# Optimization experiments

Hardware: AMD Instinct MI355X
Metric: run time of the kernel (lower is better)

## Reference

```python
import jax, jax.numpy as jnp
import numpy as np

MARGIN = 1.0  # config['margin']


def setup_inputs() -> dict:
    key = jax.random.key(0)
    k1, k2 = jax.random.split(key)
    features = jax.random.normal(k1, (1024, 512), dtype=jnp.float32)
    labels = jax.random.randint(k2, (1024,), 0, 32)
    return {"features": features, "labels": labels}


def _cdist(x):
    # Pairwise euclidean distances, matching torch.cdist; zero-distance
    # entries (e.g., the diagonal) get zero gradient like torch's backward.
    sq = jnp.sum(x * x, axis=-1)
    d2 = sq[:, None] + sq[None, :] - 2.0 * (x @ x.T)
    d2 = jnp.maximum(d2, 0.0)
    safe = jnp.where(d2 > 0.0, d2, 1.0)
    return jnp.where(d2 > 0.0, jnp.sqrt(safe), 0.0)


def reference(features, labels):
    n = features.shape[0]
    dist = _cdist(features)                                   # [N, N]
    pos = (labels[:, None] == labels[None, :]).astype(features.dtype)  # includes diagonal, as in the torch code
    neg = 1.0 - pos

    # loss = sum_i sum_{p in pos(i)} sum_{k in neg(i)} relu(d[i,p] - d[i,k] + margin)
    # Stream over anchors i to avoid materializing the [N, N, N] broadcast.
    def per_anchor(args):
        di, pi, ni = args  # each [N]
        t = jax.nn.relu(di[:, None] - di[None, :] + MARGIN)   # [N_pos_axis, N_neg_axis]
        return jnp.sum(t * (pi[:, None] * ni[None, :]))

    losses = jax.lax.map(per_anchor, (dist, pos, neg))        # [N]
    return jnp.sum(losses) / (n + 1e-8)
```

## Files before the change

kernel.cpp:

```cpp
#include <hip/hip_runtime.h>
#include <math.h>

#define MARGIN 1.0f
#define N_MAX 1024
#define BK 32
#define TSTR 68

__global__ __launch_bounds__(256) void dist_kernel(
    const float* __restrict__ f, float* __restrict__ dist, int N, int D) {
  __shared__ float As[BK][TSTR];
  __shared__ float Bs[BK][TSTR];

  const int tid = threadIdx.x;
  const int tx = tid & 15;
  const int ty = tid >> 4;
  const int rowBase = blockIdx.y * 64;
  const int colBase = blockIdx.x * 64;

  float4 aReg[2], bReg[2];

  const int r0 = tid >> 3;
  const int r1 = (tid + 256) >> 3;
  const int kc0 = (tid & 7) * 4;
  const int kc1 = kc0;

  auto loadTiles = [&](int k0) {
    aReg[0] = *(const float4*)(f + (size_t)(rowBase + r0) * D + k0 + kc0);
    aReg[1] = *(const float4*)(f + (size_t)(rowBase + r1) * D + k0 + kc1);
    bReg[0] = *(const float4*)(f + (size_t)(colBase + r0) * D + k0 + kc0);
    bReg[1] = *(const float4*)(f + (size_t)(colBase + r1) * D + k0 + kc1);
  };
  auto storeTiles = [&]() {
    As[kc0 + 0][r0] = aReg[0].x; As[kc0 + 1][r0] = aReg[0].y;
    As[kc0 + 2][r0] = aReg[0].z; As[kc0 + 3][r0] = aReg[0].w;
    As[kc1 + 0][r1] = aReg[1].x; As[kc1 + 1][r1] = aReg[1].y;
    As[kc1 + 2][r1] = aReg[1].z; As[kc1 + 3][r1] = aReg[1].w;
    Bs[kc0 + 0][r0] = bReg[0].x; Bs[kc0 + 1][r0] = bReg[0].y;
    Bs[kc0 + 2][r0] = bReg[0].z; Bs[kc0 + 3][r0] = bReg[0].w;
    Bs[kc1 + 0][r1] = bReg[1].x; Bs[kc1 + 1][r1] = bReg[1].y;
    Bs[kc1 + 2][r1] = bReg[1].z; Bs[kc1 + 3][r1] = bReg[1].w;
  };

  float c[4][4] = {};
  float asq[4] = {}, bsq[4] = {};

  loadTiles(0);
  for (int k0 = 0; k0 < D; k0 += BK) {
    __syncthreads();
    storeTiles();
    __syncthreads();
    if (k0 + BK < D) loadTiles(k0 + BK);

#pragma unroll
    for (int k = 0; k < BK; ++k) {
      float4 a = *(const float4*)&As[k][4 * ty];
      float4 b = *(const float4*)&Bs[k][4 * tx];
      float am[4] = {a.x, a.y, a.z, a.w};
      float bn[4] = {b.x, b.y, b.z, b.w};
#pragma unroll
      for (int m = 0; m < 4; ++m) asq[m] += am[m] * am[m];
#pragma unroll
      for (int n = 0; n < 4; ++n) bsq[n] += bn[n] * bn[n];
#pragma unroll
      for (int m = 0; m < 4; ++m)
#pragma unroll
        for (int n = 0; n < 4; ++n) c[m][n] += am[m] * bn[n];
    }
  }

#pragma unroll
  for (int m = 0; m < 4; ++m) {
    int row = rowBase + 4 * ty + m;
    float4 o;
    float* op = &o.x;
#pragma unroll
    for (int n = 0; n < 4; ++n) {
      float d2 = asq[m] + bsq[n] - 2.f * c[m][n];
      d2 = d2 > 0.f ? d2 : 0.f;
      op[n] = sqrtf(d2);
    }
    *(float4*)&dist[(size_t)row * N + colBase + 4 * tx] = o;
  }
}

__global__ __launch_bounds__(256) void anchor_loss_kernel(
    const float* __restrict__ dist, const int* __restrict__ labels,
    float* __restrict__ partial, int N) {
  const int i = blockIdx.x;
  const int tid = threadIdx.x;
  const int lane = tid & 63;

  __shared__ float dpos[N_MAX];
  __shared__ float dneg[N_MAX];
  __shared__ int cnt[2];
  __shared__ float red[4];

  if (tid < 2) cnt[tid] = 0;
  __syncthreads();

  const int lab = labels[i];
  const float* drow = dist + (size_t)i * N;

  for (int jb = 0; jb < N; jb += 256) {
    int j = jb + tid;
    bool valid = j < N;
    float d = valid ? drow[j] : 0.f;
    bool isPos = valid && (labels[j & (N_MAX - 1)] == lab);
    bool isNeg = valid && !isPos;

    unsigned long long mp = __ballot(isPos);
    unsigned long long mn = __ballot(isNeg);
    unsigned long long lt = (1ull << lane) - 1ull;

    int base_p = 0, base_n = 0;
    if (lane == 0) {
      base_p = atomicAdd(&cnt[0], __popcll(mp));
      base_n = atomicAdd(&cnt[1], __popcll(mn));
    }
    base_p = __shfl(base_p, 0, 64);
    base_n = __shfl(base_n, 0, 64);

    if (isPos) dpos[base_p + __popcll(mp & lt)] = d + MARGIN;
    if (isNeg) dneg[base_n + __popcll(mn & lt)] = d;
  }
  __syncthreads();

  const int np = cnt[0], nn = cnt[1];

  float dk[4];
#pragma unroll
  for (int e = 0; e < 4; ++e) {
    int k = tid + 256 * e;
    dk[e] = (k < nn) ? dneg[k] : 1e30f;
  }

  float acc = 0.f;
  for (int p = 0; p < np; ++p) {
    float t = dpos[p];
#pragma unroll
    for (int e = 0; e < 4; ++e) {
      float v = t - dk[e];
      acc += (v > 0.f) ? v : 0.f;
    }
  }

  for (int off = 32; off > 0; off >>= 1) acc += __shfl_down(acc, off, 64);
  if (lane == 0) red[tid >> 6] = acc;
  __syncthreads();
  if (tid == 0) partial[i] = red[0] + red[1] + red[2] + red[3];
}

__global__ __launch_bounds__(256) void final_reduce_kernel(
    const float* __restrict__ partial, float* __restrict__ out, int N) {
  float acc = 0.f;
  for (int j = threadIdx.x; j < N; j += 256) acc += partial[j];
  for (int off = 32; off > 0; off >>= 1) acc += __shfl_down(acc, off, 64);
  __shared__ float red[4];
  if ((threadIdx.x & 63) == 0) red[threadIdx.x >> 6] = acc;
  __syncthreads();
  if (threadIdx.x == 0) {
    double s = (double)red[0] + (double)red[1] + (double)red[2] + (double)red[3];
    out[0] = (float)(s / ((double)N + 1e-8));
  }
}

extern "C" void kernel_launch(void* const* d_in, const int* in_sizes, int n_in,
                              void* d_out, int out_size, void* d_ws, size_t ws_size,
                              hipStream_t stream) {
  const float* f = (const float*)d_in[0];
  const int* labels = (const int*)d_in[1];
  int N = in_sizes[1];
  int D = in_sizes[0] / N;
  float* out = (float*)d_out;

  float* dist = (float*)d_ws;
  float* partial = dist + (size_t)N * N;

  dim3 grid(N / 64, N / 64);
  dist_kernel<<<grid, 256, 0, stream>>>(f, dist, N, D);
  anchor_loss_kernel<<<N, 256, 0, stream>>>(dist, labels, partial, N);
  final_reduce_kernel<<<1, 256, 0, stream>>>(partial, out, N);
}
```

Baseline: 90.76 us.

## Compute pairwise distance Gram matrix with split-bf16 MFMA

Measured after the change: 85.14 us. 1.07x faster.

```diff
diff --git a/kernel.cpp b/kernel.cpp
--- a/kernel.cpp
+++ b/kernel.cpp
@@ -3,83 +3,115 @@
 
 #define MARGIN 1.0f
 #define N_MAX 1024
-#define BK 32
-#define TSTR 68
+#define BK 64
+#define LSTR 72
+
+typedef short short8 __attribute__((ext_vector_type(8)));
+typedef unsigned short ushort8 __attribute__((ext_vector_type(8)));
+typedef float floatx16 __attribute__((ext_vector_type(16)));
+
+__device__ inline unsigned short bf16_rne(float x) {
+  unsigned u = __float_as_uint(x);
+  unsigned r = (u + 0x7FFF + ((u >> 16) & 1)) >> 16;
+  return (unsigned short)r;
+}
+__device__ inline float bf16_to_f32(unsigned short h) {
+  return __uint_as_float(((unsigned)h) << 16);
+}
+
+__global__ __launch_bounds__(64) void conv_kernel(
+    const float* __restrict__ f, unsigned short* __restrict__ fhi,
+    unsigned short* __restrict__ flo, float* __restrict__ sq, int D) {
+  int row = blockIdx.x;
+  int lane = threadIdx.x;
+  const float* fr = f + (size_t)row * D;
+  unsigned short* hr = fhi + (size_t)row * D;
+  unsigned short* lr = flo + (size_t)row * D;
+
+  float acc = 0.f;
+  for (int c0 = lane * 4; c0 < D; c0 += 64 * 4) {
+    float4 v = *(const float4*)(fr + c0);
+    float xs[4] = {v.x, v.y, v.z, v.w};
+    unsigned short hs[4], ls[4];
+#pragma unroll
+    for (int e = 0; e < 4; ++e) {
+      float x = xs[e];
+      acc += x * x;
+      unsigned short h = bf16_rne(x);
+      hs[e] = h;
+      ls[e] = bf16_rne(x - bf16_to_f32(h));
+    }
+    *(ushort4*)(hr + c0) = make_ushort4(hs[0], hs[1], hs[2], hs[3]);
+    *(ushort4*)(lr + c0) = make_ushort4(ls[0], ls[1], ls[2], ls[3]);
+  }
+  for (int off = 32; off > 0; off >>= 1) acc += __shfl_down(acc, off, 64);
+  if (lane == 0) sq[row] = acc;
+}
 
 __global__ __launch_bounds__(256) void dist_kernel(
-    const float* __restrict__ f, float* __restrict__ dist, int N, int D) {
-  __shared__ float As[BK][TSTR];
-  __shared__ float Bs[BK][TSTR];
+    const unsigned short* __restrict__ fhi, const unsigned short* __restrict__ flo,
+    const float* __restrict__ sqv, float* __restrict__ dist, int N, int D) {
+  __shared__ unsigned short Ah[64][LSTR];
+  __shared__ unsigned short Al[64][LSTR];
+  __shared__ unsigned short Bh[64][LSTR];
+  __shared__ unsigned short Bl[64][LSTR];
 
   const int tid = threadIdx.x;
-  const int tx = tid & 15;
-  const int ty = tid >> 4;
   const int rowBase = blockIdx.y * 64;
   const int colBase = blockIdx.x * 64;
 
-  float4 aReg[2], bReg[2];
-
-  const int r0 = tid >> 3;
-  const int r1 = (tid + 256) >> 3;
-  const int kc0 = (tid & 7) * 4;
-  const int kc1 = kc0;
-
-  auto loadTiles = [&](int k0) {
-    aReg[0] = *(const float4*)(f + (size_t)(rowBase + r0) * D + k0 + kc0);
-    aReg[1] = *(const float4*)(f + (size_t)(rowBase + r1) * D + k0 + kc1);
-    bReg[0] = *(const float4*)(f + (size_t)(colBase + r0) * D + k0 + kc0);
-    bReg[1] = *(const float4*)(f + (size_t)(colBase + r1) * D + k0 + kc1);
-  };
-  auto storeTiles = [&]() {
-    As[kc0 + 0][r0] = aReg[0].x; As[kc0 + 1][r0] = aReg[0].y;
-    As[kc0 + 2][r0] = aReg[0].z; As[kc0 + 3][r0] = aReg[0].w;
-    As[kc1 + 0][r1] = aReg[1].x; As[kc1 + 1][r1] = aReg[1].y;
-    As[kc1 + 2][r1] = aReg[1].z; As[kc1 + 3][r1] = aReg[1].w;
-    Bs[kc0 + 0][r0] = bReg[0].x; Bs[kc0 + 1][r0] = bReg[0].y;
-    Bs[kc0 + 2][r0] = bReg[0].z; Bs[kc0 + 3][r0] = bReg[0].w;
-    Bs[kc1 + 0][r1] = bReg[1].x; Bs[kc1 + 1][r1] = bReg[1].y;
-    Bs[kc1 + 2][r1] = bReg[1].z; Bs[kc1 + 3][r1] = bReg[1].w;
-  };
-
-  float c[4][4] = {};
-  float asq[4] = {}, bsq[4] = {};
-
-  loadTiles(0);
+  const int sr = tid & 63;
+  const int sc = (tid >> 6) * 16;
+
+  const int w = tid >> 6;
+  const int lane = tid & 63;
+  const int wr = (w >> 1) * 32;
+  const int wc = (w & 1) * 32;
+  const int arow = wr + (lane & 31);
+  const int brow = wc + (lane & 31);
+  const int kgrp = (lane >> 5) * 8;
+
+  floatx16 acc = {};
+
   for (int k0 = 0; k0 < D; k0 += BK) {
+    const size_t ga = (size_t)(rowBase + sr) * D + k0 + sc;
+    const size_t gb = (size_t)(colBase + sr) * D + k0 + sc;
+    ushort8 ah0 = *(const ushort8*)(fhi + ga);
+    ushort8 ah1 = *(const ushort8*)(fhi + ga + 8);
+    ushort8 al0 = *(const ushort8*)(flo + ga);
+    ushort8 al1 = *(const ushort8*)(flo + ga + 8);
+    ushort8 bh0 = *(const ushort8*)(fhi + gb);
+    ushort8 bh1 = *(const ushort8*)(fhi + gb + 8);
+    ushort8 bl0 = *(const ushort8*)(flo + gb);
+    ushort8 bl1 = *(const ushort8*)(flo + gb + 8);
     __syncthreads();
-    storeTiles();
+    *(ushort8*)&Ah[sr][sc] = ah0; *(ushort8*)&Ah[sr][sc + 8] = ah1;
+    *(ushort8*)&Al[sr][sc] = al0; *(ushort8*)&Al[sr][sc + 8] = al1;
+    *(ushort8*)&Bh[sr][sc] = bh0; *(ushort8*)&Bh[sr][sc + 8] = bh1;
+    *(ushort8*)&Bl[sr][sc] = bl0; *(ushort8*)&Bl[sr][sc + 8] = bl1;
     __syncthreads();
-    if (k0 + BK < D) loadTiles(k0 + BK);
-
-#pragma unroll
-    for (int k = 0; k < BK; ++k) {
-      float4 a = *(const float4*)&As[k][4 * ty];
-      float4 b = *(const float4*)&Bs[k][4 * tx];
-      float am[4] = {a.x, a.y, a.z, a.w};
-      float bn[4] = {b.x, b.y, b.z, b.w};
-#pragma unroll
-      for (int m = 0; m < 4; ++m) asq[m] += am[m] * am[m];
-#pragma unroll
-      for (int n = 0; n < 4; ++n) bsq[n] += bn[n] * bn[n];
-#pragma unroll
-      for (int m = 0; m < 4; ++m)
-#pragma unroll
-        for (int n = 0; n < 4; ++n) c[m][n] += am[m] * bn[n];
-    }
-  }
-
-#pragma unroll
-  for (int m = 0; m < 4; ++m) {
-    int row = rowBase + 4 * ty + m;
-    float4 o;
-    float* op = &o.x;
-#pragma unroll
-    for (int n = 0; n < 4; ++n) {
-      float d2 = asq[m] + bsq[n] - 2.f * c[m][n];
-      d2 = d2 > 0.f ? d2 : 0.f;
-      op[n] = sqrtf(d2);
-    }
-    *(float4*)&dist[(size_t)row * N + colBase + 4 * tx] = o;
+
+#pragma unroll
+    for (int kk = 0; kk < BK / 16; ++kk) {
+      const int ko = kk * 16 + kgrp;
+      short8 ahf = *(const short8*)&Ah[arow][ko];
+      short8 alf = *(const short8*)&Al[arow][ko];
+      short8 bhf = *(const short8*)&Bh[brow][ko];
+      short8 blf = *(const short8*)&Bl[brow][ko];
+      acc = __builtin_amdgcn_mfma_f32_32x32x16_bf16(ahf, bhf, acc, 0, 0, 0);
+      acc = __builtin_amdgcn_mfma_f32_32x32x16_bf16(ahf, blf, acc, 0, 0, 0);
+      acc = __builtin_amdgcn_mfma_f32_32x32x16_bf16(alf, bhf, acc, 0, 0, 0);
+    }
+  }
+
+  const int col = colBase + wc + (lane & 31);
+  const float sqc = sqv[col];
+#pragma unroll
+  for (int r = 0; r < 16; ++r) {
+    const int row = rowBase + wr + (r & 3) + 8 * (r >> 2) + 4 * (lane >> 5);
+    float d2 = sqv[row] + sqc - 2.0f * acc[r];
+    d2 = d2 > 0.f ? d2 : 0.f;
+    dist[(size_t)row * N + col] = sqrtf(d2);
   }
 }
 
@@ -134,18 +166,18 @@
     dk[e] = (k < nn) ? dneg[k] : 1e30f;
   }
 
-  float acc = 0.f;
+  float accv = 0.f;
   for (int p = 0; p < np; ++p) {
     float t = dpos[p];
 #pragma unroll
     for (int e = 0; e < 4; ++e) {
       float v = t - dk[e];
-      acc += (v > 0.f) ? v : 0.f;
-    }
-  }
-
-  for (int off = 32; off > 0; off >>= 1) acc += __shfl_down(acc, off, 64);
-  if (lane == 0) red[tid >> 6] = acc;
+      accv += (v > 0.f) ? v : 0.f;
+    }
+  }
+
+  for (int off = 32; off > 0; off >>= 1) accv += __shfl_down(accv, off, 64);
+  if (lane == 0) red[tid >> 6] = accv;
   __syncthreads();
   if (tid == 0) partial[i] = red[0] + red[1] + red[2] + red[3];
 }
@@ -173,11 +205,15 @@
   int D = in_sizes[0] / N;
   float* out = (float*)d_out;
 
-  float* dist = (float*)d_ws;
+  unsigned short* fhi = (unsigned short*)d_ws;
+  unsigned short* flo = fhi + (size_t)N * D;
+  float* sq = (float*)(flo + (size_t)N * D);
+  float* dist = sq + N;
   float* partial = dist + (size_t)N * N;
 
+  conv_kernel<<<N, 64, 0, stream>>>(f, fhi, flo, sq, D);
   dim3 grid(N / 64, N / 64);
-  dist_kernel<<<grid, 256, 0, stream>>>(f, dist, N, D);
+  dist_kernel<<<grid, 256, 0, stream>>>(fhi, flo, sq, dist, N, D);
   anchor_loss_kernel<<<N, 256, 0, stream>>>(dist, labels, partial, N);
   final_reduce_kernel<<<1, 256, 0, stream>>>(partial, out, N);
 }
```
